# Optimization experiments

Hardware: AMD Instinct MI355X
Metric: run time of the kernel (lower is better)

Reference implementation:

```python
import jax, jax.numpy as jnp
import numpy as np

# ---- MUSIC hyperparameters (from init_kwargs) ----
N_FFT = 512
HOP = 256
FS = 16000
F_LOW = 400
F_HIGH = 1000
D_INTER = 0.1
C_SOUND = 343.0
SOURCE_NUM = 2
MIC_NUM = 4
RESOLUTION = 0.01
EST_NUM = 4      # snapshots used for spatial covariance
T_START = 120    # starting STFT frame
EPS = 1e-8
N_SAMPLES = 9_600_000

# sqrt of periodic Hann window (torch.hann_window(512).pow(0.5))
_WIN = np.sqrt(0.5 * (1.0 - np.cos(2.0 * np.pi * np.arange(N_FFT) / N_FFT))).astype(np.float32)
# analog frequency grid and static usable-bin mask
_F_ALL = np.linspace(0.0, FS / 2.0, N_FFT // 2 + 1)
_F_MASK = (_F_ALL >= F_LOW) & (_F_ALL < F_HIGH)
_F_USE = _F_ALL[_F_MASK].astype(np.float32)          # (F_use,) ~ 19 bins
_N_ANGLES = int(180 / RESOLUTION + 1)                 # 18001


def setup_inputs() -> dict:
    key = jax.random.key(0)
    x = jax.random.normal(key, (N_SAMPLES, MIC_NUM), dtype=jnp.float32)
    return {"x": x}


def _music(x):
    # x: (T_samples, C) -> multichannel STFT, center=True reflect pad (torch.stft default)
    xc = x.T                                              # (C, T)
    pad = jnp.pad(xc, ((0, 0), (N_FFT // 2, N_FFT // 2)), mode="reflect")
    n_frames = 1 + x.shape[0] // HOP
    idx = np.arange(n_frames)[:, None] * HOP + np.arange(N_FFT)  # (Tf, 512)
    frames = pad[:, idx] * jnp.asarray(_WIN)              # (C, Tf, 512)
    X = jnp.fft.rfft(frames, axis=-1)                     # (C, Tf, 257) complex64
    X = X[:, :, _F_MASK]                                  # (C, Tf, F_use)

    # spatial covariance from EST_NUM snapshots starting at T_START
    Xs = X[:, T_START:T_START + EST_NUM, :]               # (C, est, F)
    spt = jnp.einsum("ctf,dtf->fcd", Xs, jnp.conj(Xs)) / EST_NUM  # (F, C, C) Hermitian

    # noise subspace: eigenvectors of the MIC_NUM - SOURCE_NUM smallest eigenvalues
    _, V = jnp.linalg.eigh(spt)                           # ascending eigenvalues
    En = V[:, :, : MIC_NUM - SOURCE_NUM]                  # (F, C, K)

    # steering vectors for all angles at once (vectorized over the 18001-angle loop)
    theta = jnp.deg2rad(jnp.linspace(-90.0, 90.0, _N_ANGLES))
    sin_t = jnp.sin(theta).astype(jnp.float32)            # (A,)
    mic_idx = jnp.arange(MIC_NUM, dtype=jnp.float32)      # (C,)
    f_use = jnp.asarray(_F_USE)                           # (F,)
    phase = (2.0 * jnp.pi * D_INTER / C_SOUND) * sin_t[:, None, None] \
            * f_use[None, :, None] * mic_idx[None, None, :]        # (A, F, C)
    steer = jnp.exp(-1j * phase)                          # (A, F, C) complex64

    # project onto noise subspace: MUSIC pseudo-spectrum
    proj = jnp.einsum("afc,fck->afk", steer, En)          # (A, F, K)
    denom = jnp.sum(jnp.abs(proj) ** 2, axis=-1) + EPS    # (A, F)
    spt_spec = jnp.mean(1.0 / denom, axis=1)              # mean over freqs -> (A,)
    return spt_spec


def reference(x):
    return _music(x)
```

## Files before the change

### kernel.cpp

```cpp
#include <hip/hip_runtime.h>
#include <math.h>

#define HOP 256
#define T_START 120
#define NFREQ 19
#define KMIN 13
#define NANGLES 18001

__global__ __launch_bounds__(64) void k_dft(const float* __restrict__ x,
                                            double* __restrict__ ws) {
    const int blk  = blockIdx.x;
    const int k    = blk >> 4;
    const int t    = (blk >> 2) & 3;
    const int c    = blk & 3;
    const int lane = threadIdx.x;
    const int kact = KMIN + k;
    const int base = (T_START - 1 + t) * HOP;

    double xr = 0.0, xi = 0.0;
#pragma unroll
    for (int j = 0; j < 8; ++j) {
        const int n = lane + 64 * j;
        const double v = (double)x[(size_t)(base + n) * 4 + c];
        const double w = sinpi((double)n / 512.0);
        double sp, cp;
        sincospi((double)(kact * n) / 256.0, &sp, &cp);
        xr += v * w * cp;
        xi -= v * w * sp;
    }
#pragma unroll
    for (int off = 32; off > 0; off >>= 1) {
        xr += __shfl_down(xr, off, 64);
        xi += __shfl_down(xi, off, 64);
    }
    if (lane == 0) {
        ws[2 * blk]     = xr;
        ws[2 * blk + 1] = xi;
    }
}

__global__ __launch_bounds__(64) void k_eig(const double* __restrict__ wsX,
                                            double* __restrict__ tb) {
    const int f = threadIdx.x;
    if (f >= NFREQ) return;

    double Xr[4][4], Xi[4][4];
#pragma unroll
    for (int t = 0; t < 4; ++t)
#pragma unroll
        for (int c = 0; c < 4; ++c) {
            const int idx = f * 16 + t * 4 + c;
            Xr[t][c] = wsX[2 * idx];
            Xi[t][c] = wsX[2 * idx + 1];
        }

    double Ar[4][4], Ai[4][4], Vr[4][4], Vi[4][4];
#pragma unroll
    for (int a = 0; a < 4; ++a)
#pragma unroll
        for (int d = 0; d < 4; ++d) {
            double ar = 0.0, ai = 0.0;
#pragma unroll
            for (int t = 0; t < 4; ++t) {
                ar += Xr[t][a] * Xr[t][d] + Xi[t][a] * Xi[t][d];
                ai += Xi[t][a] * Xr[t][d] - Xr[t][a] * Xi[t][d];
            }
            Ar[a][d] = 0.25 * ar;
            Ai[a][d] = 0.25 * ai;
            Vr[a][d] = (a == d) ? 1.0 : 0.0;
            Vi[a][d] = 0.0;
        }

    const int PP[6] = {0, 0, 0, 1, 1, 2};
    const int QQ[6] = {1, 2, 3, 2, 3, 3};
    for (int sweep = 0; sweep < 8; ++sweep) {
#pragma unroll
        for (int r6 = 0; r6 < 6; ++r6) {
            const int p = PP[r6], q = QQ[r6];
            const double zr = Ar[p][q], zi = Ai[p][q];
            const double rr = sqrt(zr * zr + zi * zi);
            if (rr < 1e-30) continue;
            const double tau = (Ar[q][q] - Ar[p][p]) / (2.0 * rr);
            const double sq  = sqrt(tau * tau + 1.0);
            const double tt  = (tau >= 0.0) ? (-1.0 / (tau + sq)) : (1.0 / (sq - tau));
            const double cc  = 1.0 / sqrt(1.0 + tt * tt);
            const double sg  = tt * cc;
            const double inv_r = 1.0 / rr;
            const double sr =  sg * zr * inv_r;
            const double si = -sg * zi * inv_r;
#pragma unroll
            for (int kk = 0; kk < 4; ++kk) {
                const double apr = Ar[kk][p], api = Ai[kk][p];
                const double aqr = Ar[kk][q], aqi = Ai[kk][q];
                Ar[kk][p] = cc * apr + sr * aqr - si * aqi;
                Ai[kk][p] = cc * api + sr * aqi + si * aqr;
                Ar[kk][q] = cc * aqr - (sr * apr + si * api);
                Ai[kk][q] = cc * aqi - (sr * api - si * apr);
            }
#pragma unroll
            for (int kk = 0; kk < 4; ++kk) {
                const double apr = Ar[p][kk], api = Ai[p][kk];
                const double aqr = Ar[q][kk], aqi = Ai[q][kk];
                Ar[p][kk] = cc * apr + sr * aqr + si * aqi;
                Ai[p][kk] = cc * api + sr * aqi - si * aqr;
                Ar[q][kk] = cc * aqr - (sr * apr - si * api);
                Ai[q][kk] = cc * aqi - (sr * api + si * apr);
            }
#pragma unroll
            for (int kk = 0; kk < 4; ++kk) {
                const double vpr = Vr[kk][p], vpi = Vi[kk][p];
                const double vqr = Vr[kk][q], vqi = Vi[kk][q];
                Vr[kk][p] = cc * vpr + sr * vqr - si * vqi;
                Vi[kk][p] = cc * vpi + sr * vqi + si * vqr;
                Vr[kk][q] = cc * vqr - (sr * vpr + si * vpi);
                Vi[kk][q] = cc * vqi - (sr * vpi - si * vpr);
            }
        }
    }

    double dg[4] = {Ar[0][0], Ar[1][1], Ar[2][2], Ar[3][3]};
    int i0 = 0;
#pragma unroll
    for (int j = 1; j < 4; ++j)
        if (dg[j] < dg[i0]) i0 = j;
    int i1 = (i0 == 0) ? 1 : 0;
#pragma unroll
    for (int j = 0; j < 4; ++j)
        if (j != i0 && dg[j] < dg[i1]) i1 = j;

    double u0r[4], u0i[4], u1r[4], u1i[4];
#pragma unroll
    for (int c = 0; c < 4; ++c) {
        u0r[c] = Vr[c][i0]; u0i[c] = Vi[c][i0];
        u1r[c] = Vr[c][i1]; u1i[c] = Vi[c][i1];
    }

    double T0 = 0.0;
#pragma unroll
    for (int c = 0; c < 4; ++c)
        T0 += u0r[c] * u0r[c] + u0i[c] * u0i[c] + u1r[c] * u1r[c] + u1i[c] * u1i[c];
    double q1r = 0, q1i = 0, q2r = 0, q2i = 0, q3r = 0, q3i = 0;
#pragma unroll
    for (int c = 0; c < 3; ++c) {
        q1r += u0r[c] * u0r[c+1] + u0i[c] * u0i[c+1] + u1r[c] * u1r[c+1] + u1i[c] * u1i[c+1];
        q1i += u0i[c] * u0r[c+1] - u0r[c] * u0i[c+1] + u1i[c] * u1r[c+1] - u1r[c] * u1i[c+1];
    }
#pragma unroll
    for (int c = 0; c < 2; ++c) {
        q2r += u0r[c] * u0r[c+2] + u0i[c] * u0i[c+2] + u1r[c] * u1r[c+2] + u1i[c] * u1i[c+2];
        q2i += u0i[c] * u0r[c+2] - u0r[c] * u0i[c+2] + u1i[c] * u1r[c+2] - u1r[c] * u1i[c+2];
    }
    q3r = u0r[0] * u0r[3] + u0i[0] * u0i[3] + u1r[0] * u1r[3] + u1i[0] * u1i[3];
    q3i = u0i[0] * u0r[3] - u0r[0] * u0i[3] + u1i[0] * u1r[3] - u1r[0] * u1i[3];

    double* o = tb + f * 7;
    o[0] = T0;
    o[1] = q1r; o[2] = q1i;
    o[3] = q2r; o[4] = q2i;
    o[5] = q3r; o[6] = q3i;
}

__global__ __launch_bounds__(256) void k_scan(const double* __restrict__ tb_g,
                                              float* __restrict__ out) {
    __shared__ double tb[NFREQ * 7];
    if (threadIdx.x < NFREQ * 7) tb[threadIdx.x] = tb_g[threadIdx.x];
    __syncthreads();
    const int i = blockIdx.x * 256 + threadIdx.x;
    if (i >= NANGLES) return;

    const double deg = -90.0 + 0.01 * (double)i;
    const double sth = sin(deg * (M_PI / 180.0));
    const double KC  = 2.0 * M_PI * 0.1 / 343.0;
    const double a   = KC * sth;

    double c0, s0, cd, sd;
    sincos(a * (31.25 * (double)KMIN), &s0, &c0);
    sincos(a * 31.25, &sd, &cd);

    double sum = 0.0;
#pragma unroll
    for (int k = 0; k < NFREQ; ++k) {
        const double* e = &tb[7 * k];
        const double c2 = c0 * c0 - s0 * s0, s2 = 2.0 * c0 * s0;
        const double c3 = c2 * c0 - s2 * s0, s3 = s2 * c0 + c2 * s0;
        const double den = e[0]
            + 2.0 * (e[1] * c0 - e[2] * s0 + e[3] * c2 - e[4] * s2 + e[5] * c3 - e[6] * s3)
            + 1e-8;
        sum += 1.0 / den;
        const double cn = c0 * cd - s0 * sd;
        s0 = s0 * cd + c0 * sd;
        c0 = cn;
    }
    out[i] = (float)(sum * (1.0 / 19.0));
}

extern "C" void kernel_launch(void* const* d_in, const int* in_sizes, int n_in,
                              void* d_out, int out_size, void* d_ws, size_t ws_size,
                              hipStream_t stream) {
    const float* x = (const float*)d_in[0];
    double* ws = (double*)d_ws;
    float* out = (float*)d_out;

    hipLaunchKernelGGL(k_dft, dim3(NFREQ * 16), dim3(64), 0, stream, x, ws);
    hipLaunchKernelGGL(k_eig, dim3(1), dim3(64), 0, stream, ws, ws + 2 * NFREQ * 16);
    hipLaunchKernelGGL(k_scan, dim3((NANGLES + 255) / 256), dim3(256), 0, stream,
                       ws + 2 * NFREQ * 16, out);
}
```

Before: 206.8 us.

## Vectorize DFT over channels with twiddle recurrences and cut Jacobi sweeps

The DFT kernel now processes all four channels per block by loading float4 samples. It replaces per-sample sincospi calls for the window and twiddle factors with rotation recurrences, and issues a quarter as many blocks. The Jacobi eigensolver switches to a different pivot order and runs 5 sweeps instead of 8, which shortens the serial single-thread stage. The risks are accumulated rounding from the recurrences and less convergence margin from the fewer sweeps.

Result: no change. 206.4 us (-0.2%).

```diff
diff --git a/kernel.cpp b/kernel.cpp
--- a/kernel.cpp
+++ b/kernel.cpp
@@ -7,35 +7,63 @@
 #define KMIN 13
 #define NANGLES 18001
 
-__global__ __launch_bounds__(64) void k_dft(const float* __restrict__ x,
+__constant__ double C8[8] = {1.0, 0.70710678118654752, 0.0, -0.70710678118654752,
+                             -1.0, -0.70710678118654752, 0.0, 0.70710678118654752};
+__constant__ double S8[8] = {0.0, 0.70710678118654752, 1.0, 0.70710678118654752,
+                             0.0, -0.70710678118654752, -1.0, -0.70710678118654752};
+
+__global__ __launch_bounds__(64) void k_dft(const float4* __restrict__ x4,
                                             double* __restrict__ ws) {
     const int blk  = blockIdx.x;
-    const int k    = blk >> 4;
-    const int t    = (blk >> 2) & 3;
-    const int c    = blk & 3;
+    const int k    = blk >> 2;
+    const int t    = blk & 3;
     const int lane = threadIdx.x;
     const int kact = KMIN + k;
     const int base = (T_START - 1 + t) * HOP;
 
-    double xr = 0.0, xi = 0.0;
+    const double c8 = 0.98078528040323044913;
+    const double cw8 = 0.92387953251128675613;
+    const double sw8 = 0.38268343236508977173;
+    (void)c8;
+    double sw, cw;
+    sincospi((double)lane / 512.0, &sw, &cw);
+
+    double sp, cp;
+    sincospi((double)(kact * lane) / 256.0, &sp, &cp);
+    const int m = kact & 7;
+    const double cd = C8[m], sd = S8[m];
+
+    double xr0 = 0, xi0 = 0, xr1 = 0, xi1 = 0;
+    double xr2 = 0, xi2 = 0, xr3 = 0, xi3 = 0;
 #pragma unroll
     for (int j = 0; j < 8; ++j) {
-        const int n = lane + 64 * j;
-        const double v = (double)x[(size_t)(base + n) * 4 + c];
-        const double w = sinpi((double)n / 512.0);
-        double sp, cp;
-        sincospi((double)(kact * n) / 256.0, &sp, &cp);
-        xr += v * w * cp;
-        xi -= v * w * sp;
+        const float4 v = x4[base + lane + 64 * j];
+        const double wr = sw * cp;
+        const double wi = sw * sp;
+        xr0 += (double)v.x * wr;  xi0 -= (double)v.x * wi;
+        xr1 += (double)v.y * wr;  xi1 -= (double)v.y * wi;
+        xr2 += (double)v.z * wr;  xi2 -= (double)v.z * wi;
+        xr3 += (double)v.w * wr;  xi3 -= (double)v.w * wi;
+        const double nw = sw * cw8 + cw * sw8;
+        cw = cw * cw8 - sw * sw8;
+        sw = nw;
+        const double np = sp * cd + cp * sd;
+        cp = cp * cd - sp * sd;
+        sp = np;
     }
 #pragma unroll
     for (int off = 32; off > 0; off >>= 1) {
-        xr += __shfl_down(xr, off, 64);
-        xi += __shfl_down(xi, off, 64);
+        xr0 += __shfl_down(xr0, off, 64);  xi0 += __shfl_down(xi0, off, 64);
+        xr1 += __shfl_down(xr1, off, 64);  xi1 += __shfl_down(xi1, off, 64);
+        xr2 += __shfl_down(xr2, off, 64);  xi2 += __shfl_down(xi2, off, 64);
+        xr3 += __shfl_down(xr3, off, 64);  xi3 += __shfl_down(xi3, off, 64);
     }
     if (lane == 0) {
-        ws[2 * blk]     = xr;
-        ws[2 * blk + 1] = xi;
+        const int idx = k * 16 + t * 4;
+        ws[2 * (idx + 0)] = xr0;  ws[2 * (idx + 0) + 1] = xi0;
+        ws[2 * (idx + 1)] = xr1;  ws[2 * (idx + 1) + 1] = xi1;
+        ws[2 * (idx + 2)] = xr2;  ws[2 * (idx + 2) + 1] = xi2;
+        ws[2 * (idx + 3)] = xr3;  ws[2 * (idx + 3) + 1] = xi3;
     }
 }
 
@@ -71,9 +99,9 @@
             Vi[a][d] = 0.0;
         }
 
-    const int PP[6] = {0, 0, 0, 1, 1, 2};
-    const int QQ[6] = {1, 2, 3, 2, 3, 3};
-    for (int sweep = 0; sweep < 8; ++sweep) {
+    const int PP[6] = {0, 2, 0, 1, 0, 1};
+    const int QQ[6] = {1, 3, 2, 3, 3, 2};
+    for (int sweep = 0; sweep < 5; ++sweep) {
 #pragma unroll
         for (int r6 = 0; r6 < 6; ++r6) {
             const int p = PP[r6], q = QQ[r6];
@@ -197,11 +225,11 @@
 extern "C" void kernel_launch(void* const* d_in, const int* in_sizes, int n_in,
                               void* d_out, int out_size, void* d_ws, size_t ws_size,
                               hipStream_t stream) {
-    const float* x = (const float*)d_in[0];
+    const float4* x4 = (const float4*)d_in[0];
     double* ws = (double*)d_ws;
     float* out = (float*)d_out;
 
-    hipLaunchKernelGGL(k_dft, dim3(NFREQ * 16), dim3(64), 0, stream, x, ws);
+    hipLaunchKernelGGL(k_dft, dim3(NFREQ * 4), dim3(64), 0, stream, x4, ws);
     hipLaunchKernelGGL(k_eig, dim3(1), dim3(64), 0, stream, ws, ws + 2 * NFREQ * 16);
     hipLaunchKernelGGL(k_scan, dim3((NANGLES + 255) / 256), dim3(256), 0, stream,
                        ws + 2 * NFREQ * 16, out);
```
